# Optimization experiments

Measured on AMD Instinct MI355X. Metric: run time of the kernel, lower is better.

The kernel has to match this reference:

```python
import jax, jax.numpy as jnp
import numpy as np

EMBED_DIM = 1024
HEAD = 16
DK = EMBED_DIM // HEAD  # 64
B, S = 2, 2048
NEG = -1.0e9


def setup_inputs() -> dict:
    key = jax.random.key(0)
    ks = jax.random.split(key, 8)
    d = {
        'query': jax.random.normal(ks[0], (B, S, EMBED_DIM), jnp.float32),
        'key': jax.random.normal(ks[1], (B, S, EMBED_DIM), jnp.float32),
        'value': jax.random.normal(ks[2], (B, S, EMBED_DIM), jnp.float32),
        'masked': jax.random.randint(ks[3], (B, S, S), 0, 2).astype(bool),
        'Wq': jax.random.normal(ks[4], (EMBED_DIM, EMBED_DIM), jnp.float32) / np.sqrt(EMBED_DIM),
        'Wk': jax.random.normal(ks[5], (EMBED_DIM, EMBED_DIM), jnp.float32) / np.sqrt(EMBED_DIM),
        'Wv': jax.random.normal(ks[6], (EMBED_DIM, EMBED_DIM), jnp.float32) / np.sqrt(EMBED_DIM),
        'Wo': jax.random.normal(ks[7], (EMBED_DIM, EMBED_DIM), jnp.float32) / np.sqrt(EMBED_DIM),
    }
    return d


def reference(query, key, value, masked, Wq, Wk, Wv, Wo):
    # projections (bias-free Linear: x @ W), split into heads: [B, H, S, DK]
    def split_heads(x):
        b, s, _ = x.shape
        return x.reshape(b, s, HEAD, DK).transpose(0, 2, 1, 3)

    q = split_heads(query @ Wq)
    k = split_heads(key @ Wk)
    v = split_heads(value @ Wv)

    scale = 1.0 / jnp.sqrt(jnp.asarray(DK, q.dtype))
    scores = jnp.einsum('bhqd,bhkd->bhqk', q, k) * scale
    scores = jnp.where(masked[:, None, :, :], NEG, scores)
    attn = jax.nn.softmax(scores, axis=-1)
    out = jnp.einsum('bhqk,bhkd->bhqd', attn, v)  # [B, H, S, DK]
    out = out.transpose(0, 2, 1, 3).reshape(query.shape[0], -1, EMBED_DIM)
    return out @ Wo
```

## Files before the change

kernel.cpp:

```cpp
#include <hip/hip_runtime.h>
#include <hip/hip_bf16.h>

typedef float f32x4 __attribute__((ext_vector_type(4)));
typedef __bf16 bf16x8 __attribute__((ext_vector_type(8)));

__device__ __forceinline__ unsigned short f2bf(float f){
  unsigned int u = __builtin_bit_cast(unsigned int, f);
  u += 0x7fffu + ((u >> 16) & 1u);
  return (unsigned short)(u >> 16);
}
__device__ __forceinline__ float bf2f(unsigned short h){
  return __builtin_bit_cast(float, (unsigned int)h << 16);
}

__device__ __forceinline__ void glds16(const void* g, void* l){
  __builtin_amdgcn_global_load_lds((const __attribute__((address_space(1))) void*)g,
                                   (__attribute__((address_space(3))) void*)l, 16, 0, 0);
}

__device__ __forceinline__ f32x4 mfma16(bf16x8 a, bf16x8 b, f32x4 c){
  return __builtin_amdgcn_mfma_f32_16x16x32_bf16(a, b, c, 0, 0, 0);
}

#if __has_builtin(__builtin_amdgcn_exp2f)
__device__ __forceinline__ float exp2v(float x){ return __builtin_amdgcn_exp2f(x); }
#else
__device__ __forceinline__ float exp2v(float x){ return exp2f(x); }
#endif

__device__ __forceinline__ unsigned int cvtpk(float a, float b){
  unsigned int r;
  asm("v_cvt_pk_bf16_f32 %0, %1, %2" : "=v"(r) : "v"(a), "v"(b));
  return r;
}

__global__ void detect_kernel(const unsigned int* __restrict__ m, int* __restrict__ flag){
  int t = threadIdx.x;
  int bad = 0;
  for(int i = t; i < 4096; i += 256) bad |= (m[i] > 1u);
  unsigned long long b = __ballot(bad != 0);
  __shared__ int sbuf[4];
  if((t & 63) == 0) sbuf[t >> 6] = (b != 0ull);
  __syncthreads();
  if(t == 0) flag[0] = (sbuf[0] | sbuf[1] | sbuf[2] | sbuf[3]) ? 0 : 1;
}

__global__ void pack_mask_kernel(const unsigned char* __restrict__ m8,
                                 unsigned int* __restrict__ mp,
                                 const int* __restrict__ flag){
  const int wid = threadIdx.x >> 6, lane = threadIdx.x & 63;
  const int row = blockIdx.x * 4 + wid;
  const int is32 = flag[0];
  const int* m32 = (const int*)m8;
  for(int c0 = 0; c0 < 2048; c0 += 64){
    int mv = is32 ? m32[(size_t)row*2048 + c0 + lane]
                  : (int)m8[(size_t)row*2048 + c0 + lane];
    unsigned long long b = __ballot(mv != 0);
    if(lane == 0){
      mp[(size_t)row*64 + (c0 >> 5)]     = (unsigned int)b;
      mp[(size_t)row*64 + (c0 >> 5) + 1] = (unsigned int)(b >> 32);
    }
  }
}

__global__ void cvt_kernel(const float* __restrict__ src, unsigned short* __restrict__ dst){
  int i = blockIdx.x * 256 + threadIdx.x;
  const float4* s = (const float4*)src;
  float4 a = s[2*i], b = s[2*i+1];
  union { unsigned short h[8]; uint4 v; } o;
  o.h[0]=f2bf(a.x); o.h[1]=f2bf(a.y); o.h[2]=f2bf(a.z); o.h[3]=f2bf(a.w);
  o.h[4]=f2bf(b.x); o.h[5]=f2bf(b.y); o.h[6]=f2bf(b.z); o.h[7]=f2bf(b.w);
  ((uint4*)dst)[i] = o.v;
}

__global__ void transW_kernel(const float* __restrict__ Wq, const float* __restrict__ Wk,
                              const float* __restrict__ Wv, const float* __restrict__ Wo,
                              unsigned short* __restrict__ WT){
  const float* W = (blockIdx.y==0)?Wq:(blockIdx.y==1)?Wk:(blockIdx.y==2)?Wv:Wo;
  unsigned short* D = WT + (size_t)blockIdx.y * 1048576;
  int r0 = (blockIdx.x >> 4) * 64, c0 = (blockIdx.x & 15) * 64;
  __shared__ unsigned short T[64][65];
  int t = threadIdx.x;
  {
    int r = t >> 2, cb = (t & 3) * 16;
    const float4* src = (const float4*)(W + (size_t)(r0 + r) * 1024 + (c0 + cb));
    float4 v0 = src[0], v1 = src[1], v2 = src[2], v3 = src[3];
    float vals[16] = {v0.x,v0.y,v0.z,v0.w, v1.x,v1.y,v1.z,v1.w,
                      v2.x,v2.y,v2.z,v2.w, v3.x,v3.y,v3.z,v3.w};
    #pragma unroll
    for(int j=0;j<16;j++) T[cb + j][r] = f2bf(vals[j]);
  }
  __syncthreads();
  {
    int c = t >> 2, rb = (t & 3) * 16;
    union { unsigned short h[16]; uint4 v[2]; } o;
    #pragma unroll
    for(int j=0;j<16;j++) o.h[j] = T[c][rb + j];
    uint4* dp = (uint4*)(D + (size_t)(c0 + c) * 1024 + (r0 + rb));
    dp[0] = o.v[0]; dp[1] = o.v[1];
  }
}

__global__ void transV_kernel(const unsigned short* __restrict__ Vb,
                              unsigned short* __restrict__ Vt){
  const int bh = blockIdx.y, b = bh >> 4, h = bh & 15;
  const int s0 = blockIdx.x * 64;
  __shared__ unsigned short T[64][68];
  const int t = threadIdx.x;
  {
    int r = t >> 2, cb = (t & 3) * 16;
    const uint4* src = (const uint4*)(Vb + (size_t)(b*2048 + s0 + r)*1024 + h*64 + cb);
    union { unsigned short h[16]; uint4 v[2]; } o;
    o.v[0] = src[0]; o.v[1] = src[1];
    uint2* dst = (uint2*)&T[r][cb];
    const uint2* sv = (const uint2*)o.h;
    dst[0]=sv[0]; dst[1]=sv[1]; dst[2]=sv[2]; dst[3]=sv[3];
  }
  __syncthreads();
  {
    int c = t >> 2, sb = (t & 3) * 16;
    union { unsigned short h[16]; uint4 v[2]; } o;
    #pragma unroll
    for(int j=0;j<16;j++) o.h[j] = T[sb + j][c];
    uint4* dp = (uint4*)(Vt + (size_t)(bh*64 + c)*2048 + s0 + sb);
    dp[0] = o.v[0]; dp[1] = o.v[1];
  }
}

template<int OUTF32>
__global__ __launch_bounds__(256,2) void gemm_bt(
    const unsigned short* __restrict__ A0, const unsigned short* __restrict__ A1, const unsigned short* __restrict__ A2,
    const unsigned short* __restrict__ B0, const unsigned short* __restrict__ B1, const unsigned short* __restrict__ B2,
    unsigned short* __restrict__ C0, unsigned short* __restrict__ C1, unsigned short* __restrict__ C2,
    float* __restrict__ Cf)
{
  const unsigned short* A  = (blockIdx.z==0)?A0:(blockIdx.z==1)?A1:A2;
  const unsigned short* BT = (blockIdx.z==0)?B0:(blockIdx.z==1)?B1:B2;
  unsigned short* C        = (blockIdx.z==0)?C0:(blockIdx.z==1)?C1:C2;
  __shared__ unsigned short Asm[128*32];
  __shared__ unsigned short Bsm[128*32];
  const int wid = threadIdx.x >> 6, lane = threadIdx.x & 63;
  const int m0 = blockIdx.x * 128, n0 = blockIdx.y * 128;
  const int wrow = wid >> 1, wcol = wid & 1;
  f32x4 acc[4][4] = {};
  const int sr = lane >> 2;
  const int sc = lane & 3;

  for(int kt = 0; kt < 32; ++kt){
    const int kofs = kt * 32;
    #pragma unroll
    for(int i=0;i<2;i++){
      int r = wid*32 + i*16 + sr;
      int blk = sc ^ (r & 3);
      glds16(A  + (size_t)(m0 + r)*1024 + kofs + blk*8, &Asm[(wid*32 + i*16)*32]);
      glds16(BT + (size_t)(n0 + r)*1024 + kofs + blk*8, &Bsm[(wid*32 + i*16)*32]);
    }
    __syncthreads();
    bf16x8 af[4], bfv[4];
    #pragma unroll
    for(int fm=0; fm<4; fm++){
      int row = wrow*64 + fm*16 + (lane & 15);
      int blk = (lane >> 4) ^ (row & 3);
      af[fm] = *(const bf16x8*)&Asm[row*32 + blk*8];
    }
    #pragma unroll
    for(int fn=0; fn<4; fn++){
      int row = wcol*64 + fn*16 + (lane & 15);
      int blk = (lane >> 4) ^ (row & 3);
      bfv[fn] = *(const bf16x8*)&Bsm[row*32 + blk*8];
    }
    __builtin_amdgcn_s_setprio(1);
    #pragma unroll
    for(int fm=0; fm<4; fm++)
      #pragma unroll
      for(int fn=0; fn<4; fn++)
        acc[fm][fn] = mfma16(af[fm], bfv[fn], acc[fm][fn]);
    __builtin_amdgcn_s_setprio(0);
    __syncthreads();
  }
  #pragma unroll
  for(int fm=0; fm<4; fm++){
    #pragma unroll
    for(int fn=0; fn<4; fn++){
      int col  = n0 + wcol*64 + fn*16 + (lane & 15);
      int rowb = m0 + wrow*64 + fm*16 + (lane >> 4)*4;
      #pragma unroll
      for(int r=0;r<4;r++){
        if(OUTF32) Cf[(size_t)(rowb + r)*1024 + col] = acc[fm][fn][r];
        else       C [(size_t)(rowb + r)*1024 + col] = f2bf(acc[fm][fn][r]);
      }
    }
  }
}

__global__ __launch_bounds__(256,4) void attn_kernel(
    const unsigned short* __restrict__ Q, const unsigned short* __restrict__ K,
    const unsigned short* __restrict__ Vt, unsigned short* __restrict__ O,
    const unsigned int* __restrict__ mp)
{
  __shared__ unsigned short Ksm[2][64*64];
  __shared__ unsigned short Vsm[2][64*64];
  __shared__ unsigned short Psm[4][16][64];
  const int wid = threadIdx.x >> 6, lane = threadIdx.x & 63;
  const int orig = blockIdx.x;
  const int wg = (orig & 7) * 128 + (orig >> 3);
  const int qt = wg & 31, bh = wg >> 5;
  const int b = bh >> 4, h = bh & 15;
  const int q0 = qt * 64;
  const int li = lane & 15, lg = lane >> 4;

  bf16x8 qf[2];
  {
    const unsigned short* qp = Q + (size_t)(b*2048 + q0 + wid*16 + li)*1024 + h*64 + lg*8;
    union { unsigned short s[8]; bf16x8 v; } u0, u1;
    u0.v = *(const bf16x8*)qp; u1.v = *(const bf16x8*)(qp + 32);
    #pragma unroll
    for(int j=0;j<8;j++){
      u0.s[j] = f2bf(bf2f(u0.s[j]) * 0.1803368801111601f);
      u1.s[j] = f2bf(bf2f(u1.s[j]) * 0.1803368801111601f);
    }
    qf[0] = u0.v; qf[1] = u1.v;
  }

  f32x4 oacc[4] = {};
  float mrow = -__builtin_inff();
  float lrow = 0.f;

  const int srow = lane >> 3;
  const int sblk = (lane & 7) ^ srow;
  const int mrowg = b*2048 + q0 + wid*16 + li;
  const int li7 = li & 7;

  #pragma unroll
  for(int i=0;i<2;i++){
    int r = wid*16 + i*8 + srow;
    glds16(K  + (size_t)(b*2048 + r)*1024 + h*64 + sblk*8, &Ksm[0][(wid*16 + i*8)*64]);
    glds16(Vt + (size_t)(bh*64 + r)*2048 + sblk*8,         &Vsm[0][(wid*16 + i*8)*64]);
  }
  uint2 mw = *(const uint2*)&mp[(size_t)mrowg*64];
  uint2 mwn;
  __syncthreads();

  int buf = 0;
  for(int t = 0; t < 32; ++t){
    const int kv0 = t * 64;
    if(t < 31){
      #pragma unroll
      for(int i=0;i<2;i++){
        int r = wid*16 + i*8 + srow;
        glds16(K  + (size_t)(b*2048 + kv0 + 64 + r)*1024 + h*64 + sblk*8, &Ksm[buf^1][(wid*16 + i*8)*64]);
        glds16(Vt + (size_t)(bh*64 + r)*2048 + kv0 + 64 + sblk*8,         &Vsm[buf^1][(wid*16 + i*8)*64]);
      }
      mwn = *(const uint2*)&mp[(size_t)mrowg*64 + (size_t)((kv0 + 64) >> 5)];
    }
    float p[4][4];
    __builtin_amdgcn_s_setprio(1);
    #pragma unroll
    for(int f=0; f<4; f++){
      f32x4 s = {0.f,0.f,0.f,0.f};
      #pragma unroll
      for(int kf=0; kf<2; kf++){
        int blk = (kf*4 + lg) ^ li7;
        bf16x8 kfr = *(const bf16x8*)&Ksm[buf][(f*16 + li)*64 + blk*8];
        s = mfma16(kfr, qf[kf], s);
      }
      #pragma unroll
      for(int j=0;j<4;j++) p[f][j] = s[j];
    }
    __builtin_amdgcn_s_setprio(0);
    #pragma unroll
    for(int f=0; f<4; f++){
      unsigned int w = (f < 2) ? mw.x : mw.y;
      #pragma unroll
      for(int j=0;j<4;j++){
        unsigned int bit = (w >> ((f & 1)*16 + lg*4 + j)) & 1u;
        p[f][j] = bit ? -1.0e9f : p[f][j];
      }
    }
    float tmax;
    {
      float m0 = fmaxf(fmaxf(p[0][0],p[0][1]), fmaxf(p[0][2],p[0][3]));
      float m1 = fmaxf(fmaxf(p[1][0],p[1][1]), fmaxf(p[1][2],p[1][3]));
      float m2 = fmaxf(fmaxf(p[2][0],p[2][1]), fmaxf(p[2][2],p[2][3]));
      float m3 = fmaxf(fmaxf(p[3][0],p[3][1]), fmaxf(p[3][2],p[3][3]));
      tmax = fmaxf(fmaxf(m0,m1), fmaxf(m2,m3));
      tmax = fmaxf(tmax, __shfl_xor(tmax, 16));
      tmax = fmaxf(tmax, __shfl_xor(tmax, 32));
    }
    if(__any(tmax > mrow + 8.f)){
      float mn = fmaxf(mrow, tmax);
      float scal = exp2v(mrow - mn);
      mrow = mn;
      lrow *= scal;
      float so0 = __shfl(scal, lg*4 + 0);
      float so1 = __shfl(scal, lg*4 + 1);
      float so2 = __shfl(scal, lg*4 + 2);
      float so3 = __shfl(scal, lg*4 + 3);
      #pragma unroll
      for(int d=0; d<4; d++){
        oacc[d][0] *= so0; oacc[d][1] *= so1; oacc[d][2] *= so2; oacc[d][3] *= so3;
      }
    }
    {
      float rs = 0.f;
      #pragma unroll
      for(int f=0; f<4; f++){
        float e0 = exp2v(p[f][0] - mrow);
        float e1 = exp2v(p[f][1] - mrow);
        float e2 = exp2v(p[f][2] - mrow);
        float e3 = exp2v(p[f][3] - mrow);
        rs += (e0 + e1) + (e2 + e3);
        unsigned int a0 = cvtpk(e0, e1);
        unsigned int a1 = cvtpk(e2, e3);
        int blk = (f*2 + (lg >> 1)) ^ li7;
        uint2 w2; w2.x = a0; w2.y = a1;
        *(uint2*)&Psm[wid][li][blk*8 + (lg & 1)*4] = w2;
      }
      lrow += rs;
    }
    __builtin_amdgcn_s_setprio(1);
    #pragma unroll
    for(int ks=0; ks<2; ks++){
      bf16x8 pa = *(const bf16x8*)&Psm[wid][li][((ks*4 + lg) ^ li7)*8];
      #pragma unroll
      for(int d=0; d<4; d++){
        int blk = (ks*4 + lg) ^ li7;
        bf16x8 vf = *(const bf16x8*)&Vsm[buf][(d*16 + li)*64 + blk*8];
        oacc[d] = mfma16(pa, vf, oacc[d]);
      }
    }
    __builtin_amdgcn_s_setprio(0);
    __syncthreads();
    mw = mwn;
    buf ^= 1;
  }
  float rs = lrow;
  rs += __shfl_xor(rs, 16);
  rs += __shfl_xor(rs, 32);
  float inv = 1.0f / rs;
  float io0 = __shfl(inv, lg*4 + 0);
  float io1 = __shfl(inv, lg*4 + 1);
  float io2 = __shfl(inv, lg*4 + 2);
  float io3 = __shfl(inv, lg*4 + 3);
  #pragma unroll
  for(int d=0; d<4; d++){
    size_t rb = (size_t)(b*2048 + q0 + wid*16 + lg*4);
    O[(rb+0)*1024 + h*64 + 16*d + li] = f2bf(oacc[d][0] * io0);
    O[(rb+1)*1024 + h*64 + 16*d + li] = f2bf(oacc[d][1] * io1);
    O[(rb+2)*1024 + h*64 + 16*d + li] = f2bf(oacc[d][2] * io2);
    O[(rb+3)*1024 + h*64 + 16*d + li] = f2bf(oacc[d][3] * io3);
  }
}

extern "C" void kernel_launch(void* const* d_in, const int* in_sizes, int n_in,
                              void* d_out, int out_size, void* d_ws, size_t ws_size,
                              hipStream_t stream)
{
  const float* q_in = (const float*)d_in[0];
  const float* k_in = (const float*)d_in[1];
  const float* v_in = (const float*)d_in[2];
  const unsigned char* mask = (const unsigned char*)d_in[3];
  const float* Wq = (const float*)d_in[4];
  const float* Wk = (const float*)d_in[5];
  const float* Wv = (const float*)d_in[6];
  const float* Wo = (const float*)d_in[7];

  char* ws = (char*)d_ws;
  const size_t MB = 1024*1024;
  int* flag          = (int*)ws;
  unsigned short* XQ = (unsigned short*)(ws + 256);
  unsigned short* XK = (unsigned short*)(ws + 256 + 8*MB);
  unsigned short* XV = (unsigned short*)(ws + 256 + 16*MB);
  unsigned short* WT = (unsigned short*)(ws + 256 + 24*MB);
  unsigned short* Qb = (unsigned short*)(ws + 256 + 32*MB);
  unsigned short* Kb = (unsigned short*)(ws + 256 + 40*MB);
  unsigned short* Vb = (unsigned short*)(ws + 256 + 48*MB);
  unsigned short* Ob = XQ;
  unsigned short* Vt = XK;
  unsigned int*   mpk= (unsigned int*)XV;

  detect_kernel<<<1, 256, 0, stream>>>((const unsigned int*)mask, flag);
  cvt_kernel<<<2048, 256, 0, stream>>>(q_in, XQ);
  cvt_kernel<<<2048, 256, 0, stream>>>(k_in, XK);
  cvt_kernel<<<2048, 256, 0, stream>>>(v_in, XV);
  transW_kernel<<<dim3(256,4), 256, 0, stream>>>(Wq, Wk, Wv, Wo, WT);
  gemm_bt<0><<<dim3(32,8,3), 256, 0, stream>>>(XQ, XK, XV,
                                               WT, WT + 1048576, WT + 2097152,
                                               Qb, Kb, Vb, nullptr);
  transV_kernel<<<dim3(32,32), 256, 0, stream>>>(Vb, Vt);
  pack_mask_kernel<<<1024, 256, 0, stream>>>(mask, mpk, flag);
  attn_kernel<<<1024, 256, 0, stream>>>(Qb, Kb, Vt, Ob, mpk);
  gemm_bt<1><<<dim3(32,8,1), 256, 0, stream>>>(Ob, Ob, Ob,
                                               WT + 3*1048576, WT + 3*1048576, WT + 3*1048576,
                                               nullptr, nullptr, nullptr, (float*)d_out);
}
```

Before: 171.5 us.

## Rewrite attention with 32x32 MFMA tiles and register-resident P fragments

Replaces the 16x16x32 MFMA attention kernel with one using 32x32x16 MFMAs, where each wave handles 32 query rows and each block covers 128 query rows, so half as many blocks are launched. The softmax probabilities are converted to bf16 and rearranged across lanes with shuffles instead of a round trip through shared memory, and the per-row rescale and normalise factors are broadcast through a small LDS array. This is meant to raise MFMA efficiency and halve K/V tile reloads per query, at the cost of higher register pressure (launch bounds lowered to 2), fewer resident waves, and only 512 blocks to spread across the CUs.

```diff
diff --git a/kernel.cpp b/kernel.cpp
--- a/kernel.cpp
+++ b/kernel.cpp
@@ -2,6 +2,7 @@
 #include <hip/hip_bf16.h>
 
 typedef float f32x4 __attribute__((ext_vector_type(4)));
+typedef float f32x16 __attribute__((ext_vector_type(16)));
 typedef __bf16 bf16x8 __attribute__((ext_vector_type(8)));
 
 __device__ __forceinline__ unsigned short f2bf(float f){
@@ -20,6 +21,9 @@
 
 __device__ __forceinline__ f32x4 mfma16(bf16x8 a, bf16x8 b, f32x4 c){
   return __builtin_amdgcn_mfma_f32_16x16x32_bf16(a, b, c, 0, 0, 0);
+}
+__device__ __forceinline__ f32x16 mfma32(bf16x8 a, bf16x8 b, f32x16 c){
+  return __builtin_amdgcn_mfma_f32_32x32x16_bf16(a, b, c, 0, 0, 0);
 }
 
 #if __has_builtin(__builtin_amdgcn_exp2f)
@@ -193,43 +197,43 @@
   }
 }
 
-__global__ __launch_bounds__(256,4) void attn_kernel(
+__global__ __launch_bounds__(256,2) void attn32_kernel(
     const unsigned short* __restrict__ Q, const unsigned short* __restrict__ K,
     const unsigned short* __restrict__ Vt, unsigned short* __restrict__ O,
     const unsigned int* __restrict__ mp)
 {
   __shared__ unsigned short Ksm[2][64*64];
   __shared__ unsigned short Vsm[2][64*64];
-  __shared__ unsigned short Psm[4][16][64];
+  __shared__ float scalw[4][32];
   const int wid = threadIdx.x >> 6, lane = threadIdx.x & 63;
   const int orig = blockIdx.x;
-  const int wg = (orig & 7) * 128 + (orig >> 3);
-  const int qt = wg & 31, bh = wg >> 5;
+  const int wg = (orig & 7) * 64 + (orig >> 3);
+  const int qt = wg & 15, bh = wg >> 4;
   const int b = bh >> 4, h = bh & 15;
-  const int q0 = qt * 64;
-  const int li = lane & 15, lg = lane >> 4;
-
-  bf16x8 qf[2];
-  {
-    const unsigned short* qp = Q + (size_t)(b*2048 + q0 + wid*16 + li)*1024 + h*64 + lg*8;
-    union { unsigned short s[8]; bf16x8 v; } u0, u1;
-    u0.v = *(const bf16x8*)qp; u1.v = *(const bf16x8*)(qp + 32);
-    #pragma unroll
-    for(int j=0;j<8;j++){
-      u0.s[j] = f2bf(bf2f(u0.s[j]) * 0.1803368801111601f);
-      u1.s[j] = f2bf(bf2f(u1.s[j]) * 0.1803368801111601f);
-    }
-    qf[0] = u0.v; qf[1] = u1.v;
-  }
-
-  f32x4 oacc[4] = {};
+  const int q0 = qt * 128;
+  const int l31 = lane & 31, hi = lane >> 5, l7 = lane & 7;
+  const int qrow = q0 + wid*32 + l31;
+
+  bf16x8 qf[4];
+  {
+    const unsigned short* qp = Q + (size_t)(b*2048 + qrow)*1024 + h*64 + hi*8;
+    #pragma unroll
+    for(int s=0;s<4;s++){
+      union { unsigned short u[8]; bf16x8 v; } uu;
+      uu.v = *(const bf16x8*)(qp + s*16);
+      #pragma unroll
+      for(int j=0;j<8;j++) uu.u[j] = f2bf(bf2f(uu.u[j]) * 0.1803368801111601f);
+      qf[s] = uu.v;
+    }
+  }
+
+  f32x16 o0 = {}, o1 = {};
   float mrow = -__builtin_inff();
   float lrow = 0.f;
 
   const int srow = lane >> 3;
   const int sblk = (lane & 7) ^ srow;
-  const int mrowg = b*2048 + q0 + wid*16 + li;
-  const int li7 = li & 7;
+  const size_t mbase = (size_t)(b*2048 + qrow) * 64;
 
   #pragma unroll
   for(int i=0;i<2;i++){
@@ -237,7 +241,7 @@
     glds16(K  + (size_t)(b*2048 + r)*1024 + h*64 + sblk*8, &Ksm[0][(wid*16 + i*8)*64]);
     glds16(Vt + (size_t)(bh*64 + r)*2048 + sblk*8,         &Vsm[0][(wid*16 + i*8)*64]);
   }
-  uint2 mw = *(const uint2*)&mp[(size_t)mrowg*64];
+  uint2 mw = *(const uint2*)&mp[mbase];
   uint2 mwn;
   __syncthreads();
 
@@ -251,104 +255,113 @@
         glds16(K  + (size_t)(b*2048 + kv0 + 64 + r)*1024 + h*64 + sblk*8, &Ksm[buf^1][(wid*16 + i*8)*64]);
         glds16(Vt + (size_t)(bh*64 + r)*2048 + kv0 + 64 + sblk*8,         &Vsm[buf^1][(wid*16 + i*8)*64]);
       }
-      mwn = *(const uint2*)&mp[(size_t)mrowg*64 + (size_t)((kv0 + 64) >> 5)];
-    }
-    float p[4][4];
+      mwn = *(const uint2*)&mp[mbase + (size_t)((kv0 + 64) >> 5)];
+    }
+    f32x16 s0 = {}, s1 = {};
     __builtin_amdgcn_s_setprio(1);
     #pragma unroll
-    for(int f=0; f<4; f++){
-      f32x4 s = {0.f,0.f,0.f,0.f};
-      #pragma unroll
-      for(int kf=0; kf<2; kf++){
-        int blk = (kf*4 + lg) ^ li7;
-        bf16x8 kfr = *(const bf16x8*)&Ksm[buf][(f*16 + li)*64 + blk*8];
-        s = mfma16(kfr, qf[kf], s);
-      }
-      #pragma unroll
-      for(int j=0;j<4;j++) p[f][j] = s[j];
+    for(int s=0;s<4;s++){
+      int pos = (2*s + hi) ^ l7;
+      bf16x8 k0 = *(const bf16x8*)&Ksm[buf][(l31)*64      + pos*8];
+      bf16x8 k1 = *(const bf16x8*)&Ksm[buf][(32 + l31)*64 + pos*8];
+      s0 = mfma32(k0, qf[s], s0);
+      s1 = mfma32(k1, qf[s], s1);
     }
     __builtin_amdgcn_s_setprio(0);
-    #pragma unroll
-    for(int f=0; f<4; f++){
-      unsigned int w = (f < 2) ? mw.x : mw.y;
-      #pragma unroll
-      for(int j=0;j<4;j++){
-        unsigned int bit = (w >> ((f & 1)*16 + lg*4 + j)) & 1u;
-        p[f][j] = bit ? -1.0e9f : p[f][j];
+    {
+      unsigned int base0 = mw.x >> (hi*4);
+      unsigned int base1 = mw.y >> (hi*4);
+      #pragma unroll
+      for(int r=0;r<16;r++){
+        const int sh = (r&3) + 8*(r>>2);
+        s0[r] = ((base0 >> sh) & 1u) ? -1.0e9f : s0[r];
+        s1[r] = ((base1 >> sh) & 1u) ? -1.0e9f : s1[r];
       }
     }
     float tmax;
     {
-      float m0 = fmaxf(fmaxf(p[0][0],p[0][1]), fmaxf(p[0][2],p[0][3]));
-      float m1 = fmaxf(fmaxf(p[1][0],p[1][1]), fmaxf(p[1][2],p[1][3]));
-      float m2 = fmaxf(fmaxf(p[2][0],p[2][1]), fmaxf(p[2][2],p[2][3]));
-      float m3 = fmaxf(fmaxf(p[3][0],p[3][1]), fmaxf(p[3][2],p[3][3]));
-      tmax = fmaxf(fmaxf(m0,m1), fmaxf(m2,m3));
-      tmax = fmaxf(tmax, __shfl_xor(tmax, 16));
-      tmax = fmaxf(tmax, __shfl_xor(tmax, 32));
+      float a = fmaxf(s0[0], s1[0]);
+      #pragma unroll
+      for(int r=1;r<16;r++) a = fmaxf(a, fmaxf(s0[r], s1[r]));
+      tmax = fmaxf(a, __shfl_xor(a, 32));
     }
     if(__any(tmax > mrow + 8.f)){
       float mn = fmaxf(mrow, tmax);
       float scal = exp2v(mrow - mn);
       mrow = mn;
       lrow *= scal;
-      float so0 = __shfl(scal, lg*4 + 0);
-      float so1 = __shfl(scal, lg*4 + 1);
-      float so2 = __shfl(scal, lg*4 + 2);
-      float so3 = __shfl(scal, lg*4 + 3);
-      #pragma unroll
-      for(int d=0; d<4; d++){
-        oacc[d][0] *= so0; oacc[d][1] *= so1; oacc[d][2] *= so2; oacc[d][3] *= so3;
+      if(hi == 0) scalw[wid][l31] = scal;
+      asm volatile("s_waitcnt lgkmcnt(0)" ::: "memory");
+      __builtin_amdgcn_sched_barrier(0);
+      #pragma unroll
+      for(int r=0;r<16;r++){
+        float sr = scalw[wid][(r&3) + 8*(r>>2) + 4*hi];
+        o0[r] *= sr; o1[r] *= sr;
       }
     }
     {
       float rs = 0.f;
       #pragma unroll
-      for(int f=0; f<4; f++){
-        float e0 = exp2v(p[f][0] - mrow);
-        float e1 = exp2v(p[f][1] - mrow);
-        float e2 = exp2v(p[f][2] - mrow);
-        float e3 = exp2v(p[f][3] - mrow);
-        rs += (e0 + e1) + (e2 + e3);
-        unsigned int a0 = cvtpk(e0, e1);
-        unsigned int a1 = cvtpk(e2, e3);
-        int blk = (f*2 + (lg >> 1)) ^ li7;
-        uint2 w2; w2.x = a0; w2.y = a1;
-        *(uint2*)&Psm[wid][li][blk*8 + (lg & 1)*4] = w2;
+      for(int r=0;r<16;r++){
+        float e0 = exp2v(s0[r] - mrow);
+        float e1 = exp2v(s1[r] - mrow);
+        s0[r] = e0; s1[r] = e1;
+        rs += e0 + e1;
       }
       lrow += rs;
     }
+    bf16x8 pa[4];
+    {
+      #pragma unroll
+      for(int tt=0; tt<2; tt++){
+        const f32x16& e = tt ? s1 : s0;
+        #pragma unroll
+        for(int u=0; u<2; u++){
+          unsigned int y01 = cvtpk(e[u*8+0], e[u*8+1]);
+          unsigned int y23 = cvtpk(e[u*8+2], e[u*8+3]);
+          unsigned int y45 = cvtpk(e[u*8+4], e[u*8+5]);
+          unsigned int y67 = cvtpk(e[u*8+6], e[u*8+7]);
+          unsigned int t01 = __shfl_xor(y01, 32);
+          unsigned int t23 = __shfl_xor(y23, 32);
+          unsigned int t45 = __shfl_xor(y45, 32);
+          unsigned int t67 = __shfl_xor(y67, 32);
+          union { unsigned int w[4]; bf16x8 v; } fr;
+          fr.w[0] = hi ? t45 : y01;
+          fr.w[1] = hi ? t67 : y23;
+          fr.w[2] = hi ? y45 : t01;
+          fr.w[3] = hi ? y67 : t23;
+          pa[tt*2 + u] = fr.v;
+        }
+      }
+    }
     __builtin_amdgcn_s_setprio(1);
     #pragma unroll
-    for(int ks=0; ks<2; ks++){
-      bf16x8 pa = *(const bf16x8*)&Psm[wid][li][((ks*4 + lg) ^ li7)*8];
-      #pragma unroll
-      for(int d=0; d<4; d++){
-        int blk = (ks*4 + lg) ^ li7;
-        bf16x8 vf = *(const bf16x8*)&Vsm[buf][(d*16 + li)*64 + blk*8];
-        oacc[d] = mfma16(pa, vf, oacc[d]);
-      }
+    for(int s=0;s<4;s++){
+      int pos = (2*s + hi) ^ l7;
+      bf16x8 v0 = *(const bf16x8*)&Vsm[buf][(l31)*64      + pos*8];
+      bf16x8 v1 = *(const bf16x8*)&Vsm[buf][(32 + l31)*64 + pos*8];
+      o0 = mfma32(pa[s], v0, o0);
+      o1 = mfma32(pa[s], v1, o1);
     }
     __builtin_amdgcn_s_setprio(0);
     __syncthreads();
     mw = mwn;
     buf ^= 1;
   }
-  float rs = lrow;
-  rs += __shfl_xor(rs, 16);
-  rs += __shfl_xor(rs, 32);
-  float inv = 1.0f / rs;
-  float io0 = __shfl(inv, lg*4 + 0);
-  float io1 = __shfl(inv, lg*4 + 1);
-  float io2 = __shfl(inv, lg*4 + 2);
-  float io3 = __shfl(inv, lg*4 + 3);
-  #pragma unroll
-  for(int d=0; d<4; d++){
-    size_t rb = (size_t)(b*2048 + q0 + wid*16 + lg*4);
-    O[(rb+0)*1024 + h*64 + 16*d + li] = f2bf(oacc[d][0] * io0);
-    O[(rb+1)*1024 + h*64 + 16*d + li] = f2bf(oacc[d][1] * io1);
-    O[(rb+2)*1024 + h*64 + 16*d + li] = f2bf(oacc[d][2] * io2);
-    O[(rb+3)*1024 + h*64 + 16*d + li] = f2bf(oacc[d][3] * io3);
+  {
+    float rs = lrow + __shfl_xor(lrow, 32);
+    float inv = 1.0f / rs;
+    if(hi == 0) scalw[wid][l31] = inv;
+    asm volatile("s_waitcnt lgkmcnt(0)" ::: "memory");
+    __builtin_amdgcn_sched_barrier(0);
+    #pragma unroll
+    for(int r=0;r<16;r++){
+      const int qr = (r&3) + 8*(r>>2) + 4*hi;
+      float iv = scalw[wid][qr];
+      size_t row = (size_t)(b*2048 + q0 + wid*32 + qr);
+      O[row*1024 + h*64 +      l31] = f2bf(o0[r] * iv);
+      O[row*1024 + h*64 + 32 + l31] = f2bf(o1[r] * iv);
+    }
   }
 }
 
@@ -389,7 +402,7 @@
                                                Qb, Kb, Vb, nullptr);
   transV_kernel<<<dim3(32,32), 256, 0, stream>>>(Vb, Vt);
   pack_mask_kernel<<<1024, 256, 0, stream>>>(mask, mpk, flag);
-  attn_kernel<<<1024, 256, 0, stream>>>(Qb, Kb, Vt, Ob, mpk);
+  attn32_kernel<<<512, 256, 0, stream>>>(Qb, Kb, Vt, Ob, mpk);
   gemm_bt<1><<<dim3(32,8,1), 256, 0, stream>>>(Ob, Ob, Ob,
                                                WT + 3*1048576, WT + 3*1048576, WT + 3*1048576,
                                                nullptr, nullptr, nullptr, (float*)d_out);
```

Result: slower. 176.2 us (+2.7%).
